# Kernel optimization log

Hardware: AMD Instinct MI355X
Metric: run time of the kernel (lower is better)

## Reference

```python
import jax, jax.numpy as jnp
import numpy as np

B, H, D = 128, 64, 64  # batch, num_heads, head_dim; einsum structure forces seq n == m == D and H == D


def setup_inputs() -> dict:
    rng = jax.random.key(0)
    ks = jax.random.split(rng, 6)
    query = jax.random.normal(ks[0], (B, H, D, D), jnp.float32)
    key = jax.random.normal(ks[1], (B, H, D, D), jnp.float32) * 0.02
    value = jax.random.normal(ks[2], (B, H, D, D), jnp.float32) * 0.02
    memory_key = jax.random.normal(ks[3], (H, D, D), jnp.float32) * 0.02
    memory_norm = jax.random.uniform(ks[4], (H,), jnp.float32)
    memory_value = jax.random.normal(ks[5], (H, D, D), jnp.float32) * 0.02
    compression_rate = jnp.ones((H,), jnp.float32)
    return {"query": query, "key": key, "value": value,
            "memory_key": memory_key, "memory_norm": memory_norm,
            "memory_value": memory_value, "compression_rate": compression_rate}


def reference(query, key, value, memory_key, memory_norm, memory_value, compression_rate):
    h = memory_norm.shape[0]
    d = memory_key.shape[-1]

    # ---- update(key, value): associative binding + running stats (torch no_grad block) ----
    # binding in fp16 then cast to fp32, exactly as the source einsum does
    binding = jnp.einsum('bhnd,bhmd->bhnm',
                         key.astype(jnp.float16),
                         value.astype(jnp.float16)).astype(jnp.float32)
    mean_binding = binding.reshape(-1, h).mean(axis=0)            # [H] (row-major flatten, as torch .view)
    k_flat = key.reshape(-1, h, d)                                # [B*N, H, D]
    v_flat = value.reshape(-1, h, d)
    mean_value = v_flat.mean(axis=0)                              # [H, D]
    mean_key_norm = jnp.linalg.norm(k_flat.mean(axis=0), axis=-1) # [H]
    # source resets memory_key to zeros [H, D] (shape check always fires), then addcmul_
    new_memory_key = mean_binding[:, None] * mean_value           # [H, D]
    new_memory_norm = memory_norm + mean_key_norm                 # [H]
    # conditional adaptive compression
    factor = jnp.where(new_memory_norm.mean() > 0.9, compression_rate,
                       jnp.ones_like(compression_rate))
    new_memory_key = jax.lax.stop_gradient(new_memory_key * factor[:, None])
    new_memory_norm = jax.lax.stop_gradient(new_memory_norm * factor)

    # ---- retrieve(query): normalized linear-attention readout ----
    scores = jnp.einsum('bhnd,hnm->bhmd',
                        query.astype(jnp.float16),
                        memory_key.astype(jnp.float16)).astype(jnp.float32)
    # source broadcasts memory_norm [H] over the trailing dim (valid since H == D)
    scores = scores / (memory_norm + 1e-6)
    memory_output = jnp.einsum('bhmd,hnm->bhnd', scores, memory_value)
    return memory_output, scores, new_memory_key, new_memory_norm
```

## Files before the change

### kernel.cpp

```cpp
#include <hip/hip_runtime.h>
#include <hip/hip_fp16.h>

typedef _Float16 f16x8 __attribute__((ext_vector_type(8)));
typedef _Float16 f16x4 __attribute__((ext_vector_type(4)));
typedef float f32x4 __attribute__((ext_vector_type(4)));

__device__ __forceinline__ f32x4 ntld4(const float* p) {
    return __builtin_nontemporal_load((const f32x4*)p);
}
__device__ __forceinline__ float ntld1(const float* p) {
    return __builtin_nontemporal_load(p);
}
__device__ __forceinline__ f32x4 ld4(const float* p) {
    return *(const f32x4*)p;
}
__device__ __forceinline__ void st4(float* p, f32x4 v) {
    *(f32x4*)p = v;
}

__global__ __launch_bounds__(256) void mega(
    const float* __restrict__ q,   const float* __restrict__ key,
    const float* __restrict__ val, const float* __restrict__ mk,
    const float* __restrict__ mnorm, const float* __restrict__ mv,
    float* __restrict__ out_mo, float* __restrict__ out_sc,
    float* __restrict__ skp, float* __restrict__ svp, float* __restrict__ pbp,
    const int nbR)
{
    __shared__ union SM {
        struct { _Float16 qT[64][72]; _Float16 mkT[64][72]; } f;
        struct { float ktile[64][68]; float red[256]; float ks[64]; } r;
    } sm;

    const int t   = threadIdx.x;
    const int bid = blockIdx.x;

    if (bid < nbR) {
        const int r0 = t >> 4;
        const int c0 = (t & 15) << 2;
        f32x4 ska[4] = {}; f32x4 sva[4] = {};
        float pba[4] = {0.f, 0.f, 0.f, 0.f};
        f32x4 ka[4], va[4];
        int i = bid;
#pragma unroll
        for (int qq = 0; qq < 4; ++qq) {
            const int row = r0 + 16 * qq;
            ka[qq] = ntld4(key + (size_t)i * 4096 + row * 64 + c0);
            va[qq] = ntld4(val + (size_t)i * 4096 + row * 64 + c0);
        }
        while (true) {
            const int inx = i + nbR;
            const bool more = (inx < 8192);
            f32x4 kn4[4], vn4[4];
            if (more) {
#pragma unroll
                for (int qq = 0; qq < 4; ++qq) {
                    const int row = r0 + 16 * qq;
                    kn4[qq] = ntld4(key + (size_t)inx * 4096 + row * 64 + c0);
                    vn4[qq] = ntld4(val + (size_t)inx * 4096 + row * 64 + c0);
                }
            }
#pragma unroll
            for (int qq = 0; qq < 4; ++qq) {
                const int row = r0 + 16 * qq;
                ska[qq] += ka[qq];
                sva[qq] += va[qq];
                *(f32x4*)&sm.r.ktile[row][c0] = ka[qq];
            }
            __syncthreads();
            {
                const int d  = t & 63;
                const int rr = (t >> 6) * 16;
                float p = 0.f;
#pragma unroll
                for (int r = 0; r < 16; ++r) p += sm.r.ktile[rr + r][d];
                sm.r.red[t] = p;
            }
            __syncthreads();
            if (t < 64)
                sm.r.ks[t] = sm.r.red[t] + sm.r.red[t + 64] + sm.r.red[t + 128] + sm.r.red[t + 192];
            __syncthreads();
#pragma unroll
            for (int qq = 0; qq < 4; ++qq) {
                float pq = va[qq][0] * sm.r.ks[c0]     + va[qq][1] * sm.r.ks[c0 + 1]
                         + va[qq][2] * sm.r.ks[c0 + 2] + va[qq][3] * sm.r.ks[c0 + 3];
                pq += __shfl_xor(pq, 1);
                pq += __shfl_xor(pq, 2);
                pq += __shfl_xor(pq, 4);
                pq += __shfl_xor(pq, 8);
                pba[qq] += pq;
            }
            if (!more) break;
#pragma unroll
            for (int qq = 0; qq < 4; ++qq) { ka[qq] = kn4[qq]; va[qq] = vn4[qq]; }
            i = inx;
        }
        const size_t pb4 = (size_t)bid * 4096;
#pragma unroll
        for (int qq = 0; qq < 4; ++qq) {
            *(f32x4*)(skp + pb4 + 4 * t + 1024 * qq) = ska[qq];
            *(f32x4*)(svp + pb4 + 4 * t + 1024 * qq) = sva[qq];
        }
        if ((t & 15) == 0) {
#pragma unroll
            for (int qq = 0; qq < 4; ++qq)
                pbp[bid * 64 + r0 + 16 * qq] = pba[qq];
        }
        return;
    }

    const int fid = bid - nbR;
    const int h   = fid >> 7;
    const int b   = fid & 127;
    const int bh  = b * 64 + h;
    const float* qb  = q  + (size_t)bh * 4096;
    const float* mkb = mk + h * 4096;
    const float* mvb = mv + h * 4096;

    const int w  = t >> 6;
    const int l  = t & 63;
    const int lr = l & 15;
    const int lk = l >> 4;
    const size_t gbase = (size_t)bh * 4096;

    {
        const int d  = t & 63;
        const int n0 = (t >> 6) * 16;
#pragma unroll
        for (int half = 0; half < 2; ++half) {
            const int nh = n0 + 8 * half;
            float qv[8], kv[8];
#pragma unroll
            for (int i = 0; i < 8; ++i) qv[i] = ntld1(qb + (nh + i) * 64 + d);
#pragma unroll
            for (int i = 0; i < 8; ++i) kv[i] = mkb[(nh + i) * 64 + d];
            f16x8 qh, kh;
#pragma unroll
            for (int i = 0; i < 8; ++i) { qh[i] = (_Float16)qv[i]; kh[i] = (_Float16)kv[i]; }
            *(f16x8*)&sm.f.qT [d][nh] = qh;
            *(f16x8*)&sm.f.mkT[d][nh] = kh;
        }
    }
    __syncthreads();

    f32x4 acc[4] = {};
#pragma unroll
    for (int kn = 0; kn < 2; ++kn) {
        f16x8 bfr = *(const f16x8*)&sm.f.mkT[16 * w + lr][kn * 32 + lk * 8];
#pragma unroll
        for (int di = 0; di < 4; ++di) {
            f16x8 afr = *(const f16x8*)&sm.f.qT[16 * di + lr][kn * 32 + lk * 8];
            acc[di] = __builtin_amdgcn_mfma_f32_16x16x32_f16(afr, bfr, acc[di], 0, 0, 0);
        }
    }
    __syncthreads();

    f32x4 mva[4];
    {
        const float* rowp = mvb + (16 * w + lr) * 64 + lk * 8;
        mva[0] = ld4(rowp);      mva[1] = ld4(rowp + 4);
        mva[2] = ld4(rowp + 32); mva[3] = ld4(rowp + 36);
    }

    _Float16* sT = &sm.f.qT[0][0];
    const int m = 16 * w + lr;
#pragma unroll
    for (int di = 0; di < 4; ++di) {
        const int d0 = 16 * di + 4 * lk;
        f32x4 nv = ld4(mnorm + d0);
        f32x4 sv;
#pragma unroll
        for (int r = 0; r < 4; ++r) {
            sv[r] = acc[di][r] * __builtin_amdgcn_rcpf(nv[r] + 1e-6f);
            sT[(d0 + r) * 72 + m] = (_Float16)sv[r];
        }
        st4(out_sc + gbase + (size_t)m * 64 + d0, sv);
    }
    __syncthreads();

    f16x8 b2[2];
#pragma unroll
    for (int kn = 0; kn < 2; ++kn) {
        f16x8 vv;
#pragma unroll
        for (int j = 0; j < 4; ++j) {
            vv[j]     = (_Float16)mva[2 * kn][j];
            vv[j + 4] = (_Float16)mva[2 * kn + 1][j];
        }
        b2[kn] = vv;
    }
    f32x4 acc2[4] = {};
#pragma unroll
    for (int kn = 0; kn < 2; ++kn) {
#pragma unroll
        for (int di = 0; di < 4; ++di) {
            f16x8 afr = *(const f16x8*)(sT + (16 * di + lr) * 72 + kn * 32 + lk * 8);
            acc2[di] = __builtin_amdgcn_mfma_f32_16x16x32_f16(afr, b2[kn], acc2[di], 0, 0, 0);
        }
    }
#pragma unroll
    for (int di = 0; di < 4; ++di) {
        const int d0 = 16 * di + 4 * lk;
        f32x4 ov;
#pragma unroll
        for (int r = 0; r < 4; ++r) ov[r] = acc2[di][r];
        st4(out_mo + gbase + (size_t)m * 64 + d0, ov);
    }
}

#define NCHUNK 8
__global__ __launch_bounds__(256) void reduce2(
    const float* __restrict__ skp, const float* __restrict__ svp,
    const float* __restrict__ pbp, float* __restrict__ p2,
    const int nbR, const int clen)
{
    const int bi = blockIdx.x;
    const int c  = bi / 33;
    const int e  = (bi % 33) * 256 + threadIdx.x;
    if (e >= 8256) return;
    int n0 = c * clen;
    int n1 = n0 + clen; if (n1 > nbR) n1 = nbR;
    float s = 0.f;
    if (e < 4096) {
        for (int n = n0; n < n1; ++n) s += skp[(size_t)n * 4096 + e];
    } else if (e < 8192) {
        const int e2 = e - 4096;
        for (int n = n0; n < n1; ++n) s += svp[(size_t)n * 4096 + e2];
    } else {
        const int e2 = e - 8192;
        for (int n = n0; n < n1; ++n) s += pbp[n * 64 + e2];
    }
    p2[c * 8256 + e] = s;
}

__global__ __launch_bounds__(256) void finalize(
    const float* __restrict__ p2, const float* __restrict__ mnorm,
    const float* __restrict__ crate,
    float* __restrict__ out_nmk, float* __restrict__ out_nmn)
{
    __shared__ float tot[8256];
    __shared__ float fac_s[64];
    const int t = threadIdx.x;
    for (int e = t; e < 8256; e += 256) {
        float s = 0.f;
#pragma unroll
        for (int c = 0; c < NCHUNK; ++c) s += p2[c * 8256 + e];
        tot[e] = s;
    }
    __syncthreads();
    const float* sk_tot = tot;
    const float* sv_tot = tot + 4096;
    const float* pb_tot = tot + 8192;
    if (t < 64) {
        float ss = 0.f;
#pragma unroll 8
        for (int d = 0; d < 64; ++d) {
            float mkm = sk_tot[t * 64 + d] * (1.0f / 8192.0f);
            ss += mkm * mkm;
        }
        const float nmn = mnorm[t] + sqrtf(ss);
        float v = nmn;
        for (int off = 32; off; off >>= 1) v += __shfl_xor(v, off);
        const float mean = v * (1.0f / 64.0f);
        const float f = (mean > 0.9f) ? crate[t] : 1.0f;
        fac_s[t] = f;
        out_nmn[t] = nmn * f;
    }
    __syncthreads();
    for (int e = t; e < 4096; e += 256) {
        const int j = e >> 6;
        const float mb = pb_tot[j] * (1.0f / 524288.0f);
        const float mvv = sv_tot[e] * (1.0f / 8192.0f);
        out_nmk[e] = mb * mvv * fac_s[j];
    }
}

extern "C" void kernel_launch(void* const* d_in, const int* in_sizes, int n_in,
                              void* d_out, int out_size, void* d_ws, size_t ws_size,
                              hipStream_t stream) {
    const float* q  = (const float*)d_in[0];
    const float* k  = (const float*)d_in[1];
    const float* v  = (const float*)d_in[2];
    const float* mk = (const float*)d_in[3];
    const float* mn = (const float*)d_in[4];
    const float* mv = (const float*)d_in[5];
    const float* cr = (const float*)d_in[6];

    float* out     = (float*)d_out;
    float* out_mo  = out;
    float* out_sc  = out + 33554432;
    float* out_nmk = out + 67108864;
    float* out_nmn = out + 67112960;

    float* ws   = (float*)d_ws;
    float* p2   = ws;
    float* part = ws + NCHUNK * 8256;
    const size_t wsf = ws_size / 4;
    const size_t used = NCHUNK * 8256;
    const size_t avail = (wsf > used) ? (wsf - used) : 0;
    int nb = (int)(avail / 8256);
    if (nb > 512) nb = 512;
    if (nb < 1)   nb = 1;
    float* skp = part;
    float* svp = part + (size_t)nb * 4096;
    float* pbp = svp  + (size_t)nb * 4096;
    const int clen = (nb + NCHUNK - 1) / NCHUNK;

    hipLaunchKernelGGL(mega, dim3(nb + 8192), dim3(256), 0, stream,
                       q, k, v, mk, mn, mv, out_mo, out_sc, skp, svp, pbp, nb);
    hipLaunchKernelGGL(reduce2, dim3(33 * NCHUNK), dim3(256), 0, stream,
                       skp, svp, pbp, p2, nb, clen);
    hipLaunchKernelGGL(finalize, dim3(1), dim3(256), 0, stream,
                       p2, mn, cr, out_nmk, out_nmn);
}
```

Baseline: 161.5 us.

## Process four batches per block, reuse memory tiles and prefetch next query

Each forward block now handles four batch entries for one head instead of one. The memory_key and memory_value tiles and the normalization reciprocals are loaded and converted once into shared memory and reused across the four iterations. The next query tile is prefetched into registers while the current MFMA runs. This cuts redundant memory-matrix loads and block launch overhead, at the cost of more shared memory, a minimum-occupancy launch bound, and fewer blocks in the grid.

```diff
diff --git a/kernel.cpp b/kernel.cpp
--- a/kernel.cpp
+++ b/kernel.cpp
@@ -18,7 +18,7 @@
     *(f32x4*)p = v;
 }
 
-__global__ __launch_bounds__(256) void mega(
+__global__ __launch_bounds__(256, 5) void mega(
     const float* __restrict__ q,   const float* __restrict__ key,
     const float* __restrict__ val, const float* __restrict__ mk,
     const float* __restrict__ mnorm, const float* __restrict__ mv,
@@ -27,7 +27,7 @@
     const int nbR)
 {
     __shared__ union SM {
-        struct { _Float16 qT[64][72]; _Float16 mkT[64][72]; } f;
+        struct { _Float16 qT[64][72]; _Float16 mkT[64][72]; _Float16 mvs[64][72]; } f;
         struct { float ktile[64][68]; float red[256]; float ks[64]; } r;
     } sm;
 
@@ -108,11 +108,9 @@
         return;
     }
 
-    const int fid = bid - nbR;
-    const int h   = fid >> 7;
-    const int b   = fid & 127;
-    const int bh  = b * 64 + h;
-    const float* qb  = q  + (size_t)bh * 4096;
+    const int j     = bid - nbR;
+    const int h     = j >> 5;
+    const int bslot = j & 31;
     const float* mkb = mk + h * 4096;
     const float* mvb = mv + h * 4096;
 
@@ -120,90 +118,117 @@
     const int l  = t & 63;
     const int lr = l & 15;
     const int lk = l >> 4;
-    const size_t gbase = (size_t)bh * 4096;
+    const int d  = t & 63;
+    const int n0 = (t >> 6) * 16;
 
     {
-        const int d  = t & 63;
-        const int n0 = (t >> 6) * 16;
-#pragma unroll
-        for (int half = 0; half < 2; ++half) {
-            const int nh = n0 + 8 * half;
-            float qv[8], kv[8];
-#pragma unroll
-            for (int i = 0; i < 8; ++i) qv[i] = ntld1(qb + (nh + i) * 64 + d);
-#pragma unroll
-            for (int i = 0; i < 8; ++i) kv[i] = mkb[(nh + i) * 64 + d];
-            f16x8 qh, kh;
-#pragma unroll
-            for (int i = 0; i < 8; ++i) { qh[i] = (_Float16)qv[i]; kh[i] = (_Float16)kv[i]; }
-            *(f16x8*)&sm.f.qT [d][nh] = qh;
-            *(f16x8*)&sm.f.mkT[d][nh] = kh;
-        }
-    }
-    __syncthreads();
-
-    f32x4 acc[4] = {};
-#pragma unroll
-    for (int kn = 0; kn < 2; ++kn) {
-        f16x8 bfr = *(const f16x8*)&sm.f.mkT[16 * w + lr][kn * 32 + lk * 8];
-#pragma unroll
-        for (int di = 0; di < 4; ++di) {
-            f16x8 afr = *(const f16x8*)&sm.f.qT[16 * di + lr][kn * 32 + lk * 8];
-            acc[di] = __builtin_amdgcn_mfma_f32_16x16x32_f16(afr, bfr, acc[di], 0, 0, 0);
-        }
-    }
-    __syncthreads();
-
-    f32x4 mva[4];
+        float kv[16];
+#pragma unroll
+        for (int i = 0; i < 16; ++i) kv[i] = mkb[(n0 + i) * 64 + d];
+        f16x8 kh0, kh1;
+#pragma unroll
+        for (int i = 0; i < 8; ++i) { kh0[i] = (_Float16)kv[i]; kh1[i] = (_Float16)kv[i + 8]; }
+        *(f16x8*)&sm.f.mkT[d][n0]     = kh0;
+        *(f16x8*)&sm.f.mkT[d][n0 + 8] = kh1;
+
+        const int nn = t >> 2;
+        const int m0 = (t & 3) * 16;
+        f32x4 a0 = ld4(mvb + nn * 64 + m0);
+        f32x4 a1 = ld4(mvb + nn * 64 + m0 + 4);
+        f32x4 a2 = ld4(mvb + nn * 64 + m0 + 8);
+        f32x4 a3 = ld4(mvb + nn * 64 + m0 + 12);
+        f16x8 v0, v1;
+#pragma unroll
+        for (int i = 0; i < 4; ++i) {
+            v0[i] = (_Float16)a0[i]; v0[i + 4] = (_Float16)a1[i];
+            v1[i] = (_Float16)a2[i]; v1[i + 4] = (_Float16)a3[i];
+        }
+        *(f16x8*)&sm.f.mvs[nn][m0]     = v0;
+        *(f16x8*)&sm.f.mvs[nn][m0 + 8] = v1;
+    }
+
+    f32x4 scl[4];
+#pragma unroll
+    for (int di = 0; di < 4; ++di) {
+        f32x4 nv = ld4(mnorm + 16 * di + 4 * lk);
+        f32x4 s;
+#pragma unroll
+        for (int r = 0; r < 4; ++r) s[r] = __builtin_amdgcn_rcpf(nv[r] + 1e-6f);
+        scl[di] = s;
+    }
+
+    float qv[16];
     {
-        const float* rowp = mvb + (16 * w + lr) * 64 + lk * 8;
-        mva[0] = ld4(rowp);      mva[1] = ld4(rowp + 4);
-        mva[2] = ld4(rowp + 32); mva[3] = ld4(rowp + 36);
+        const float* qb = q + ((size_t)bslot * 64 + h) * 4096;
+#pragma unroll
+        for (int i = 0; i < 16; ++i) qv[i] = ntld1(qb + (n0 + i) * 64 + d);
     }
 
     _Float16* sT = &sm.f.qT[0][0];
     const int m = 16 * w + lr;
-#pragma unroll
-    for (int di = 0; di < 4; ++di) {
-        const int d0 = 16 * di + 4 * lk;
-        f32x4 nv = ld4(mnorm + d0);
-        f32x4 sv;
-#pragma unroll
-        for (int r = 0; r < 4; ++r) {
-            sv[r] = acc[di][r] * __builtin_amdgcn_rcpf(nv[r] + 1e-6f);
-            sT[(d0 + r) * 72 + m] = (_Float16)sv[r];
-        }
-        st4(out_sc + gbase + (size_t)m * 64 + d0, sv);
-    }
-    __syncthreads();
-
-    f16x8 b2[2];
-#pragma unroll
-    for (int kn = 0; kn < 2; ++kn) {
-        f16x8 vv;
-#pragma unroll
-        for (int j = 0; j < 4; ++j) {
-            vv[j]     = (_Float16)mva[2 * kn][j];
-            vv[j + 4] = (_Float16)mva[2 * kn + 1][j];
-        }
-        b2[kn] = vv;
-    }
-    f32x4 acc2[4] = {};
-#pragma unroll
-    for (int kn = 0; kn < 2; ++kn) {
+
+    for (int it = 0; it < 4; ++it) {
+        const size_t gbase = ((size_t)(bslot + 32 * it) * 64 + h) * 4096;
+
+        {
+            f16x8 qh0, qh1;
+#pragma unroll
+            for (int i = 0; i < 8; ++i) { qh0[i] = (_Float16)qv[i]; qh1[i] = (_Float16)qv[i + 8]; }
+            *(f16x8*)&sm.f.qT[d][n0]     = qh0;
+            *(f16x8*)&sm.f.qT[d][n0 + 8] = qh1;
+        }
+        __syncthreads();
+
+        f32x4 acc[4] = {};
+#pragma unroll
+        for (int kn = 0; kn < 2; ++kn) {
+            f16x8 bfr = *(const f16x8*)&sm.f.mkT[16 * w + lr][kn * 32 + lk * 8];
+#pragma unroll
+            for (int di = 0; di < 4; ++di) {
+                f16x8 afr = *(const f16x8*)&sm.f.qT[16 * di + lr][kn * 32 + lk * 8];
+                acc[di] = __builtin_amdgcn_mfma_f32_16x16x32_f16(afr, bfr, acc[di], 0, 0, 0);
+            }
+        }
+
+        if (it < 3) {
+            const float* qbn = q + ((size_t)(bslot + 32 * (it + 1)) * 64 + h) * 4096;
+#pragma unroll
+            for (int i = 0; i < 16; ++i) qv[i] = ntld1(qbn + (n0 + i) * 64 + d);
+        }
+        __syncthreads();
+
 #pragma unroll
         for (int di = 0; di < 4; ++di) {
-            f16x8 afr = *(const f16x8*)(sT + (16 * di + lr) * 72 + kn * 32 + lk * 8);
-            acc2[di] = __builtin_amdgcn_mfma_f32_16x16x32_f16(afr, b2[kn], acc2[di], 0, 0, 0);
-        }
-    }
-#pragma unroll
-    for (int di = 0; di < 4; ++di) {
-        const int d0 = 16 * di + 4 * lk;
-        f32x4 ov;
-#pragma unroll
-        for (int r = 0; r < 4; ++r) ov[r] = acc2[di][r];
-        st4(out_mo + gbase + (size_t)m * 64 + d0, ov);
+            const int d0 = 16 * di + 4 * lk;
+            f32x4 sv;
+#pragma unroll
+            for (int r = 0; r < 4; ++r) {
+                sv[r] = acc[di][r] * scl[di][r];
+                sT[(d0 + r) * 72 + m] = (_Float16)sv[r];
+            }
+            st4(out_sc + gbase + (size_t)m * 64 + d0, sv);
+        }
+        __syncthreads();
+
+        f32x4 acc2[4] = {};
+#pragma unroll
+        for (int kn = 0; kn < 2; ++kn) {
+            f16x8 bfr = *(const f16x8*)&sm.f.mvs[16 * w + lr][kn * 32 + lk * 8];
+#pragma unroll
+            for (int di = 0; di < 4; ++di) {
+                f16x8 afr = *(const f16x8*)(sT + (16 * di + lr) * 72 + kn * 32 + lk * 8);
+                acc2[di] = __builtin_amdgcn_mfma_f32_16x16x32_f16(afr, bfr, acc2[di], 0, 0, 0);
+            }
+        }
+#pragma unroll
+        for (int di = 0; di < 4; ++di) {
+            const int d0 = 16 * di + 4 * lk;
+            f32x4 ov;
+#pragma unroll
+            for (int r = 0; r < 4; ++r) ov[r] = acc2[di][r];
+            st4(out_mo + gbase + (size_t)m * 64 + d0, ov);
+        }
+        __syncthreads();
     }
 }
 
@@ -253,8 +278,8 @@
     if (t < 64) {
         float ss = 0.f;
 #pragma unroll 8
-        for (int d = 0; d < 64; ++d) {
-            float mkm = sk_tot[t * 64 + d] * (1.0f / 8192.0f);
+        for (int dd = 0; dd < 64; ++dd) {
+            float mkm = sk_tot[t * 64 + dd] * (1.0f / 8192.0f);
             ss += mkm * mkm;
         }
         const float nmn = mnorm[t] + sqrtf(ss);
@@ -267,10 +292,10 @@
     }
     __syncthreads();
     for (int e = t; e < 4096; e += 256) {
-        const int j = e >> 6;
-        const float mb = pb_tot[j] * (1.0f / 524288.0f);
+        const int jh = e >> 6;
+        const float mb = pb_tot[jh] * (1.0f / 524288.0f);
         const float mvv = sv_tot[e] * (1.0f / 8192.0f);
-        out_nmk[e] = mb * mvv * fac_s[j];
+        out_nmk[e] = mb * mvv * fac_s[jh];
     }
 }
 
@@ -305,7 +330,7 @@
     float* pbp = svp  + (size_t)nb * 4096;
     const int clen = (nb + NCHUNK - 1) / NCHUNK;
 
-    hipLaunchKernelGGL(mega, dim3(nb + 8192), dim3(256), 0, stream,
+    hipLaunchKernelGGL(mega, dim3(nb + 2048), dim3(256), 0, stream,
                        q, k, v, mk, mn, mv, out_mo, out_sc, skp, svp, pbp, nb);
     hipLaunchKernelGGL(reduce2, dim3(33 * NCHUNK), dim3(256), 0, stream,
                        skp, svp, pbp, p2, nb, clen);
```

After: 198.2 us. +22.7%, slower.
